# Kernel tuning notes

Hardware: AMD Instinct MI355X
Metric: run time of the kernel (lower is better)

Reference implementation:

```python
import jax, jax.numpy as jnp
import numpy as np

N_EMBD = 2048
N_HEAD = 16
HEAD_DIM = N_EMBD // N_HEAD
B, T = 4, 2048
EPS = 1e-5


def layer_norm(x, w, b):
    mu = jnp.mean(x, axis=-1, keepdims=True)
    var = jnp.var(x, axis=-1, keepdims=True)
    return (x - mu) * jax.lax.rsqrt(var + EPS) * w + b


def setup_inputs() -> dict:
    key = jax.random.key(0)
    ks = jax.random.split(key, 8)
    s = 0.02
    return {
        "x": jax.random.normal(ks[0], (B, T, N_EMBD), dtype=jnp.float32),
        "ln1_w": jnp.ones((N_EMBD,), jnp.float32),
        "ln1_b": jnp.zeros((N_EMBD,), jnp.float32),
        "attn_w": jax.random.normal(ks[1], (N_EMBD, 3 * N_EMBD), jnp.float32) * s,
        "attn_b": jnp.zeros((3 * N_EMBD,), jnp.float32),
        "ln2_w": jnp.ones((N_EMBD,), jnp.float32),
        "ln2_b": jnp.zeros((N_EMBD,), jnp.float32),
        "fc_w": jax.random.normal(ks[2], (N_EMBD, 4 * N_EMBD), jnp.float32) * s,
        "fc_b": jnp.zeros((4 * N_EMBD,), jnp.float32),
        "proj_w": jax.random.normal(ks[3], (4 * N_EMBD, N_EMBD), jnp.float32) * s,
        "proj_b": jnp.zeros((N_EMBD,), jnp.float32),
    }


def reference(x, ln1_w, ln1_b, attn_w, attn_b, ln2_w, ln2_b, fc_w, fc_b, proj_w, proj_b):
    b, t, c = x.shape
    # --- causal self-attention on ln_1(x); note: source Block has NO residual
    # and attention's c_proj is never invoked in the original forward. ---
    h = layer_norm(x, ln1_w, ln1_b)
    qkv = h @ attn_w + attn_b                      # [B,T,3C]
    q, k, v = jnp.split(qkv, 3, axis=-1)
    q = q.reshape(b, t, N_HEAD, HEAD_DIM)
    k = k.reshape(b, t, N_HEAD, HEAD_DIM)
    v = v.reshape(b, t, N_HEAD, HEAD_DIM)
    scale = 1.0 / np.sqrt(HEAD_DIM).astype(np.float32)
    scores = jnp.einsum("bqhd,bkhd->bhqk", q, k) * scale   # [B,H,T,T]
    causal = jnp.tril(jnp.ones((t, t), dtype=bool))
    scores = jnp.where(causal, scores, -jnp.inf)
    attn = jax.nn.softmax(scores, axis=-1)
    y = jnp.einsum("bhqk,bkhd->bqhd", attn, v).reshape(b, t, c)
    # --- MLP on ln_2(y); again no residual in the source Block ---
    h2 = layer_norm(y, ln2_w, ln2_b)
    out = jax.nn.gelu(h2 @ fc_w + fc_b, approximate=False) @ proj_w + proj_b
    return out
```

## Files before the change

kernel.cpp:

```cpp
#include <hip/hip_runtime.h>
#include <hip/hip_bf16.h>

typedef __attribute__((ext_vector_type(8))) short      bf16x8;
typedef __attribute__((ext_vector_type(4))) float      f32x4;
typedef __attribute__((ext_vector_type(8))) unsigned short u16x8;

__device__ __forceinline__ unsigned short f2bf(float f) {
    union { __hip_bfloat16 h; unsigned short u; } cv;
    cv.h = __float2bfloat16(f);
    return cv.u;
}
__device__ __forceinline__ float bf2f(unsigned short u) {
    union { float f; unsigned int i; } cv;
    cv.i = ((unsigned int)u) << 16;
    return cv.f;
}
__device__ __forceinline__ void gload_lds16(const void* g, void* l) {
    __builtin_amdgcn_global_load_lds(
        (const __attribute__((address_space(1))) void*)g,
        (__attribute__((address_space(3))) void*)l, 16, 0, 0);
}
__device__ __forceinline__ f32x4 mfma16(bf16x8 a, bf16x8 b, f32x4 c) {
    return __builtin_amdgcn_mfma_f32_16x16x32_bf16(a, b, c, 0, 0, 0);
}
__device__ __forceinline__ float gelu_f(float x) {
    return 0.5f * x * (1.0f + erff(x * 0.70710678118654752f));
}

#define VMCNT(N)  asm volatile("s_waitcnt vmcnt(" #N ")" ::: "memory")

template<int IN_BF16>
__global__ __launch_bounds__(256) void ln_kernel(const void* in, const float* w, const float* b,
                                                 unsigned short* out) {
    const int row = blockIdx.x;
    const int tid = threadIdx.x;
    float v[8];
    if constexpr (IN_BF16) {
        const unsigned short* p = (const unsigned short*)in + (size_t)row * 2048 + tid * 8;
        u16x8 raw = *(const u16x8*)p;
#pragma unroll
        for (int j = 0; j < 8; j++) v[j] = bf2f(raw[j]);
    } else {
        const float* p = (const float*)in + (size_t)row * 2048 + tid * 8;
        float4 a = ((const float4*)p)[0];
        float4 c = ((const float4*)p)[1];
        v[0] = a.x; v[1] = a.y; v[2] = a.z; v[3] = a.w;
        v[4] = c.x; v[5] = c.y; v[6] = c.z; v[7] = c.w;
    }
    float s = 0.f, ss = 0.f;
#pragma unroll
    for (int j = 0; j < 8; j++) { s += v[j]; ss += v[j] * v[j]; }
#pragma unroll
    for (int off = 32; off > 0; off >>= 1) {
        s  += __shfl_xor(s, off);
        ss += __shfl_xor(ss, off);
    }
    __shared__ float red[8];
    const int wid = tid >> 6, lane = tid & 63;
    if (lane == 0) { red[wid] = s; red[4 + wid] = ss; }
    __syncthreads();
    s  = red[0] + red[1] + red[2] + red[3];
    ss = red[4] + red[5] + red[6] + red[7];
    const float mean = s * (1.0f / 2048.0f);
    const float var  = ss * (1.0f / 2048.0f) - mean * mean;
    const float rstd = rsqrtf(var + 1e-5f);
    unsigned short* op = out + (size_t)row * 2048 + tid * 8;
    u16x8 ov;
#pragma unroll
    for (int j = 0; j < 8; j++) {
        int c = tid * 8 + j;
        ov[j] = f2bf((v[j] - mean) * rstd * w[c] + b[c]);
    }
    *(u16x8*)op = ov;
}

__global__ __launch_bounds__(256) void wt_kernel(const float* W, unsigned short* WT, int K, int N) {
    __shared__ unsigned short sm[32][33];
    const int n0 = blockIdx.x * 32, k0 = blockIdx.y * 32;
    const int tx = threadIdx.x, ty = threadIdx.y;
#pragma unroll
    for (int i = 0; i < 4; i++) {
        int k = ty + i * 8;
        sm[k][tx] = f2bf(W[(size_t)(k0 + k) * N + n0 + tx]);
    }
    __syncthreads();
#pragma unroll
    for (int i = 0; i < 4; i++) {
        int n = ty + i * 8;
        WT[(size_t)(n0 + n) * K + k0 + tx] = sm[tx][n];
    }
}

__global__ __launch_bounds__(256) void vt_kernel(const unsigned short* qkv, unsigned short* vT) {
    __shared__ unsigned short sm[32][33];
    const int t0 = blockIdx.x * 32, d0 = blockIdx.y * 32, bh = blockIdx.z;
    const int b = bh >> 4, h = bh & 15;
    const int tx = threadIdx.x, ty = threadIdx.y;
#pragma unroll
    for (int i = 0; i < 4; i++) {
        int t = ty + i * 8;
        sm[t][tx] = qkv[(size_t)(b * 2048 + t0 + t) * 6144 + 4096 + h * 128 + d0 + tx];
    }
    __syncthreads();
#pragma unroll
    for (int i = 0; i < 4; i++) {
        int d = ty + i * 8;
        vT[(size_t)(bh * 128 + d0 + d) * 2048 + t0 + tx] = sm[tx][d];
    }
}

template<int OUT_BF16, int ACT_GELU>
__global__ __launch_bounds__(512, 2) void gemm256(const unsigned short* __restrict__ A,
                                                  const unsigned short* __restrict__ BT,
                                                  const float* __restrict__ bias,
                                                  void* __restrict__ Cout,
                                                  int M, int N, int K) {
    __shared__ unsigned short As[2][256 * 64];
    __shared__ unsigned short Bs[2][256 * 64];
    const int tid = threadIdx.x;
    const int gx = gridDim.x;
    const int lin = blockIdx.y * gx + blockIdx.x;
    const int cpx = (gx * gridDim.y) >> 3;
    const int swz = (lin & 7) * cpx + (lin >> 3);
    const int n0 = (swz % gx) * 256, m0 = (swz / gx) * 256;

    const int wid = tid >> 6, lane = tid & 63;
    const int wr = wid >> 2, wc = wid & 3;
    const int lg = lane >> 4, l15 = lane & 15;
    const int nkt = K >> 6;

    const int sr = tid >> 3;
    const int scol = ((tid & 7) ^ (sr & 7)) * 8;
    const int sdst = tid * 8;

    auto stageA = [&](int ta, int h) {
        const unsigned short* g = A + (size_t)(m0 + h * 128 + sr) * K + ta * 64 + scol;
        unsigned short* d = &As[ta & 1][h * 8192 + sdst];
        gload_lds16(g, d);
        gload_lds16(g + (size_t)64 * K, d + 4096);
    };
    auto stageB = [&](int ta, int h) {
        const unsigned short* g = BT + (size_t)(n0 + h * 128 + sr) * K + ta * 64 + scol;
        unsigned short* d = &Bs[ta & 1][h * 8192 + sdst];
        gload_lds16(g, d);
        gload_lds16(g + (size_t)64 * K, d + 4096);
    };

    stageA(0, 0); stageA(0, 1); stageB(0, 0); stageB(0, 1);
    stageB(1, 0);
    VMCNT(2);
    __builtin_amdgcn_s_barrier();

    f32x4 acc[8][4] = {};
    const int lxor = l15 & 7;
    const int co0 = (lg ^ lxor) * 8;
    const int co1 = ((4 + lg) ^ lxor) * 8;
    const int aoff = wr * 8192;
    const int boff = (wc >> 1) * 8192 + (wc & 1) * 4096;

#define RD_A(P, MB, CO)                                                          \
    _Pragma("unroll") for (int i = 0; i < 4; i++)                                \
        af[i] = *(const bf16x8*)&P[aoff + (((MB) + i) * 16 + l15) * 64 + (CO)];
#define RD_B(DST, P, CO)                                                         \
    _Pragma("unroll") for (int n = 0; n < 4; n++)                                \
        DST[n] = *(const bf16x8*)&P[boff + (n * 16 + l15) * 64 + (CO)];
#define MM(MB, BQ)                                                               \
    __builtin_amdgcn_s_setprio(1);                                               \
    _Pragma("unroll") for (int i = 0; i < 4; i++)                                \
        _Pragma("unroll") for (int n = 0; n < 4; n++)                            \
            acc[(MB) + i][n] = mfma16(af[i], BQ[n], acc[(MB) + i][n]);           \
    __builtin_amdgcn_s_setprio(0);
#define BAR()  __builtin_amdgcn_s_barrier()
#define LGKM() asm volatile("s_waitcnt lgkmcnt(0)" ::: "memory")

    for (int it = 0, nit = nkt >> 1; it < nit; ++it) {
        const int T0 = it * 2, T1 = T0 + 1;
        const unsigned short* Ae = As[0];
        const unsigned short* Be = Bs[0];
        const unsigned short* Ao = As[1];
        const unsigned short* Bo = Bs[1];
        bf16x8 af[4], bq0[4], bq1[4];

        RD_A(Ae, 0, co0); RD_B(bq0, Be, co0);
        stageB(T1, 1);
        BAR(); LGKM(); MM(0, bq0); BAR();
        RD_A(Ae, 4, co0);
        stageA(T1, 0);
        BAR(); LGKM(); MM(4, bq0); BAR();
        RD_A(Ae, 0, co1); RD_B(bq1, Be, co1);
        stageA(T1, 1);
        BAR(); LGKM(); MM(0, bq1); BAR();
        RD_A(Ae, 4, co1);
        if (T0 + 2 < nkt) stageB(T0 + 2, 0);
        BAR(); LGKM(); MM(4, bq1); VMCNT(2); BAR();
        RD_A(Ao, 0, co0); RD_B(bq0, Bo, co0);
        if (T0 + 2 < nkt) stageB(T0 + 2, 1);
        BAR(); LGKM(); MM(0, bq0); BAR();
        RD_A(Ao, 4, co0);
        if (T0 + 2 < nkt) stageA(T0 + 2, 0);
        BAR(); LGKM(); MM(4, bq0); BAR();
        RD_A(Ao, 0, co1); RD_B(bq1, Bo, co1);
        if (T0 + 2 < nkt) stageA(T0 + 2, 1);
        BAR(); LGKM(); MM(0, bq1); BAR();
        RD_A(Ao, 4, co1);
        if (T1 + 2 < nkt) stageB(T1 + 2, 0);
        BAR(); LGKM(); MM(4, bq1); VMCNT(2); BAR();
    }
#undef RD_A
#undef RD_B
#undef MM
#undef BAR
#undef LGKM

#pragma unroll
    for (int n = 0; n < 4; n++) {
        const int col = n0 + wc * 64 + n * 16 + l15;
        const float bv = bias[col];
#pragma unroll
        for (int m = 0; m < 8; m++) {
            const int rbase = m0 + wr * 128 + m * 16 + lg * 4;
#pragma unroll
            for (int r = 0; r < 4; r++) {
                float v = acc[m][n][r] + bv;
                if (ACT_GELU) v = gelu_f(v);
                if (OUT_BF16)
                    ((unsigned short*)Cout)[(size_t)(rbase + r) * N + col] = f2bf(v);
                else
                    ((float*)Cout)[(size_t)(rbase + r) * N + col] = v;
            }
        }
    }
}

__global__ __launch_bounds__(256) void attn_kernel(const unsigned short* __restrict__ qkv,
                                                   const unsigned short* __restrict__ vT,
                                                   unsigned short* __restrict__ y) {
    __shared__ unsigned short Qs[64 * 128];
    __shared__ unsigned short Ks[64 * 128];
    __shared__ unsigned short VTs[128 * 64];
    const int pair = blockIdx.x, h = blockIdx.y, b = blockIdx.z;
    const int tid = threadIdx.x, wid = tid >> 6, lane = tid & 63;
    const int lg = lane >> 4, l15 = lane & 15;
    const float scale = 0.08838834764831845f;
    unsigned short* Ps = &Qs[wid * 1024];

    for (int pass = 0; pass < 2; pass++) {
        const int qt = (pass == 0) ? (31 - pair) : pair;
        __syncthreads();
#pragma unroll
        for (int i = 0; i < 4; i++) {
            int idx = tid + 256 * i;
            int row = idx >> 4, ch = idx & 15;
            const unsigned short* g = qkv + (size_t)(b * 2048 + qt * 64 + row) * 6144
                                      + h * 128 + ((ch ^ (row & 7)) * 8);
            gload_lds16(g, &Qs[idx * 8]);
        }
        __syncthreads();
        const int rq = wid * 16 + l15;
        bf16x8 qf[4];
#pragma unroll
        for (int c = 0; c < 4; c++)
            qf[c] = *(const bf16x8*)&Qs[rq * 128 + (((c * 4 + lg) ^ (rq & 7)) * 8)];

        float m_run[4], l_run[4];
#pragma unroll
        for (int r = 0; r < 4; r++) { m_run[r] = -1e30f; l_run[r] = 0.f; }
        f32x4 O[8] = {};

        const int nkb = qt + 1;
        for (int kb = 0; kb < nkb; kb++) {
            __syncthreads();
#pragma unroll
            for (int i = 0; i < 4; i++) {
                int idx = tid + 256 * i;
                int row = idx >> 4, ch = idx & 15;
                const unsigned short* g = qkv + (size_t)(b * 2048 + kb * 64 + row) * 6144
                                          + 2048 + h * 128 + ((ch ^ (row & 7)) * 8);
                gload_lds16(g, &Ks[idx * 8]);
            }
#pragma unroll
            for (int i = 0; i < 4; i++) {
                int idx = tid + 256 * i;
                int row = idx >> 3, ch = idx & 7;
                const unsigned short* g = vT + (size_t)((b * 16 + h) * 128 + row) * 2048
                                          + kb * 64 + ((ch ^ (row & 7)) * 8);
                gload_lds16(g, &VTs[idx * 8]);
            }
            __syncthreads();

            f32x4 S[4] = {};
#pragma unroll
            for (int n = 0; n < 4; n++) {
                const int rk = n * 16 + l15;
#pragma unroll
                for (int c = 0; c < 4; c++) {
                    bf16x8 kf = *(const bf16x8*)&Ks[rk * 128 + (((c * 4 + lg) ^ (rk & 7)) * 8)];
                    S[n] = mfma16(qf[c], kf, S[n]);
                }
            }

            const int qgb = qt * 64 + wid * 16 + lg * 4;
#pragma unroll
            for (int r = 0; r < 4; r++) {
                const int qg = qgb + r;
                float sv[4];
#pragma unroll
                for (int n = 0; n < 4; n++) {
                    const int kg = kb * 64 + n * 16 + l15;
                    sv[n] = (kg <= qg) ? S[n][r] * scale : -1e30f;
                }
                float mx = fmaxf(fmaxf(sv[0], sv[1]), fmaxf(sv[2], sv[3]));
                mx = fmaxf(mx, __shfl_xor(mx, 1));
                mx = fmaxf(mx, __shfl_xor(mx, 2));
                mx = fmaxf(mx, __shfl_xor(mx, 4));
                mx = fmaxf(mx, __shfl_xor(mx, 8));
                const float mnew = fmaxf(m_run[r], mx);
                const float f = __expf(m_run[r] - mnew);
                const float p0 = __expf(sv[0] - mnew), p1 = __expf(sv[1] - mnew);
                const float p2 = __expf(sv[2] - mnew), p3 = __expf(sv[3] - mnew);
                float rs = (p0 + p1) + (p2 + p3);
                rs += __shfl_xor(rs, 1);
                rs += __shfl_xor(rs, 2);
                rs += __shfl_xor(rs, 4);
                rs += __shfl_xor(rs, 8);
                l_run[r] = l_run[r] * f + rs;
                m_run[r] = mnew;
#pragma unroll
                for (int n2 = 0; n2 < 8; n2++) O[n2][r] *= f;
                const int prow = lg * 4 + r;
                const int pxor = (prow & 7) << 3;
                Ps[(prow * 64 + l15) ^ pxor]      = f2bf(p0);
                Ps[(prow * 64 + 16 + l15) ^ pxor] = f2bf(p1);
                Ps[(prow * 64 + 32 + l15) ^ pxor] = f2bf(p2);
                Ps[(prow * 64 + 48 + l15) ^ pxor] = f2bf(p3);
            }

#pragma unroll
            for (int kk = 0; kk < 2; kk++) {
                bf16x8 pf = *(const bf16x8*)&Ps[l15 * 64 + (((kk * 4 + lg) ^ (l15 & 7)) * 8)];
#pragma unroll
                for (int n2 = 0; n2 < 8; n2++) {
                    const int rv = n2 * 16 + l15;
                    bf16x8 vf = *(const bf16x8*)&VTs[rv * 64 + (((kk * 4 + lg) ^ (rv & 7)) * 8)];
                    O[n2] = mfma16(pf, vf, O[n2]);
                }
            }
        }

#pragma unroll
        for (int r = 0; r < 4; r++) {
            const float inv = 1.0f / l_run[r];
            const size_t row = (size_t)(b * 2048 + qt * 64 + wid * 16 + lg * 4 + r);
#pragma unroll
            for (int n2 = 0; n2 < 8; n2++)
                y[row * 2048 + h * 128 + n2 * 16 + l15] = f2bf(O[n2][r] * inv);
        }
    }
}

extern "C" void kernel_launch(void* const* d_in, const int* in_sizes, int n_in,
                              void* d_out, int out_size, void* d_ws, size_t ws_size,
                              hipStream_t stream) {
    const float* x      = (const float*)d_in[0];
    const float* ln1_w  = (const float*)d_in[1];
    const float* ln1_b  = (const float*)d_in[2];
    const float* attn_w = (const float*)d_in[3];
    const float* attn_b = (const float*)d_in[4];
    const float* ln2_w  = (const float*)d_in[5];
    const float* ln2_b  = (const float*)d_in[6];
    const float* fc_w   = (const float*)d_in[7];
    const float* fc_b   = (const float*)d_in[8];
    const float* proj_w = (const float*)d_in[9];
    const float* proj_b = (const float*)d_in[10];
    float* out = (float*)d_out;

    char* ws = (char*)d_ws;
    const size_t MB = 1024ull * 1024ull;
    unsigned short* Wt   = (unsigned short*)(ws + 0);
    unsigned short* X1   = (unsigned short*)(ws + 32 * MB);
    unsigned short* X2   = (unsigned short*)(ws + 64 * MB);
    unsigned short* QKV  = (unsigned short*)(ws + 96 * MB);
    unsigned short* VT   = (unsigned short*)(ws + 192 * MB);
    unsigned short* Abuf = (unsigned short*)(ws + 96 * MB);

    ln_kernel<0><<<8192, 256, 0, stream>>>(x, ln1_w, ln1_b, X1);
    wt_kernel<<<dim3(6144 / 32, 2048 / 32), dim3(32, 8), 0, stream>>>(attn_w, Wt, 2048, 6144);
    gemm256<1, 0><<<dim3(24, 32), 512, 0, stream>>>(X1, Wt, attn_b, QKV, 8192, 6144, 2048);
    vt_kernel<<<dim3(64, 4, 64), dim3(32, 8), 0, stream>>>(QKV, VT);
    attn_kernel<<<dim3(16, 16, 4), 256, 0, stream>>>(QKV, VT, X2);
    ln_kernel<1><<<8192, 256, 0, stream>>>(X2, ln2_w, ln2_b, X1);
    wt_kernel<<<dim3(8192 / 32, 2048 / 32), dim3(32, 8), 0, stream>>>(fc_w, Wt, 2048, 8192);
    gemm256<1, 1><<<dim3(32, 32), 512, 0, stream>>>(X1, Wt, fc_b, Abuf, 8192, 8192, 2048);
    wt_kernel<<<dim3(2048 / 32, 8192 / 32), dim3(32, 8), 0, stream>>>(proj_w, Wt, 8192, 2048);
    gemm256<0, 0><<<dim3(8, 32), 512, 0, stream>>>(Abuf, Wt, proj_b, out, 8192, 2048, 8192);
}
```

Before: 1.075 ms.

## Simplify GEMM main loop to one barrier per K-tile double buffering

Replaces the finely interleaved 8-phase pipeline, which staged quarter tiles between per-subtile MFMA groups with a barrier around each, with a simple loop. Each K-tile now issues the full next-tile prefetch up front, runs all MFMAs from LDS, then waits on vmcnt(0) and takes a single barrier. This drops many barriers per iteration. The cost is coarser overlap of global-to-LDS loads with compute, a full vmcnt(0) drain each tile, and LDS reads no longer fenced by explicit waits before MFMAs.

```diff
diff --git a/kernel.cpp b/kernel.cpp
--- a/kernel.cpp
+++ b/kernel.cpp
@@ -28,6 +28,8 @@
 }
 
 #define VMCNT(N)  asm volatile("s_waitcnt vmcnt(" #N ")" ::: "memory")
+#define LGKM()    asm volatile("s_waitcnt lgkmcnt(0)" ::: "memory")
+#define BAR()     __builtin_amdgcn_s_barrier()
 
 template<int IN_BF16>
 __global__ __launch_bounds__(256) void ln_kernel(const void* in, const float* w, const float* b,
@@ -131,25 +133,23 @@
 
     const int sr = tid >> 3;
     const int scol = ((tid & 7) ^ (sr & 7)) * 8;
-    const int sdst = tid * 8;
 
     auto stageA = [&](int ta, int h) {
         const unsigned short* g = A + (size_t)(m0 + h * 128 + sr) * K + ta * 64 + scol;
-        unsigned short* d = &As[ta & 1][h * 8192 + sdst];
+        unsigned short* d = &As[ta & 1][h * 8192 + tid * 8];
         gload_lds16(g, d);
         gload_lds16(g + (size_t)64 * K, d + 4096);
     };
     auto stageB = [&](int ta, int h) {
         const unsigned short* g = BT + (size_t)(n0 + h * 128 + sr) * K + ta * 64 + scol;
-        unsigned short* d = &Bs[ta & 1][h * 8192 + sdst];
+        unsigned short* d = &Bs[ta & 1][h * 8192 + tid * 8];
         gload_lds16(g, d);
         gload_lds16(g + (size_t)64 * K, d + 4096);
     };
 
     stageA(0, 0); stageA(0, 1); stageB(0, 0); stageB(0, 1);
-    stageB(1, 0);
-    VMCNT(2);
-    __builtin_amdgcn_s_barrier();
+    VMCNT(0);
+    BAR();
 
     f32x4 acc[8][4] = {};
     const int lxor = l15 & 7;
@@ -161,56 +161,36 @@
 #define RD_A(P, MB, CO)                                                          \
     _Pragma("unroll") for (int i = 0; i < 4; i++)                                \
         af[i] = *(const bf16x8*)&P[aoff + (((MB) + i) * 16 + l15) * 64 + (CO)];
-#define RD_B(DST, P, CO)                                                         \
+#define RD_B(P, CO)                                                              \
     _Pragma("unroll") for (int n = 0; n < 4; n++)                                \
-        DST[n] = *(const bf16x8*)&P[boff + (n * 16 + l15) * 64 + (CO)];
-#define MM(MB, BQ)                                                               \
+        bq[n] = *(const bf16x8*)&P[boff + (n * 16 + l15) * 64 + (CO)];
+#define MM(MB)                                                                   \
     __builtin_amdgcn_s_setprio(1);                                               \
-    _Pragma("unroll") for (int i = 0; i < 4; i++)                                \
+    _Pragma("unroll") for (int i = 0; i < 4; i++) {                              \
         _Pragma("unroll") for (int n = 0; n < 4; n++)                            \
-            acc[(MB) + i][n] = mfma16(af[i], BQ[n], acc[(MB) + i][n]);           \
+            acc[(MB) + i][n] = mfma16(af[i], bq[n], acc[(MB) + i][n]);           \
+    }                                                                            \
     __builtin_amdgcn_s_setprio(0);
-#define BAR()  __builtin_amdgcn_s_barrier()
-#define LGKM() asm volatile("s_waitcnt lgkmcnt(0)" ::: "memory")
-
-    for (int it = 0, nit = nkt >> 1; it < nit; ++it) {
-        const int T0 = it * 2, T1 = T0 + 1;
-        const unsigned short* Ae = As[0];
-        const unsigned short* Be = Bs[0];
-        const unsigned short* Ao = As[1];
-        const unsigned short* Bo = Bs[1];
-        bf16x8 af[4], bq0[4], bq1[4];
-
-        RD_A(Ae, 0, co0); RD_B(bq0, Be, co0);
-        stageB(T1, 1);
-        BAR(); LGKM(); MM(0, bq0); BAR();
-        RD_A(Ae, 4, co0);
-        stageA(T1, 0);
-        BAR(); LGKM(); MM(4, bq0); BAR();
-        RD_A(Ae, 0, co1); RD_B(bq1, Be, co1);
-        stageA(T1, 1);
-        BAR(); LGKM(); MM(0, bq1); BAR();
-        RD_A(Ae, 4, co1);
-        if (T0 + 2 < nkt) stageB(T0 + 2, 0);
-        BAR(); LGKM(); MM(4, bq1); VMCNT(2); BAR();
-        RD_A(Ao, 0, co0); RD_B(bq0, Bo, co0);
-        if (T0 + 2 < nkt) stageB(T0 + 2, 1);
-        BAR(); LGKM(); MM(0, bq0); BAR();
-        RD_A(Ao, 4, co0);
-        if (T0 + 2 < nkt) stageA(T0 + 2, 0);
-        BAR(); LGKM(); MM(4, bq0); BAR();
-        RD_A(Ao, 0, co1); RD_B(bq1, Bo, co1);
-        if (T0 + 2 < nkt) stageA(T0 + 2, 1);
-        BAR(); LGKM(); MM(0, bq1); BAR();
-        RD_A(Ao, 4, co1);
-        if (T1 + 2 < nkt) stageB(T1 + 2, 0);
-        BAR(); LGKM(); MM(4, bq1); VMCNT(2); BAR();
+
+    for (int t = 0; t < nkt; ++t) {
+        const unsigned short* Ap = As[t & 1];
+        const unsigned short* Bp = Bs[t & 1];
+        if (t + 1 < nkt) {
+            stageA(t + 1, 0); stageA(t + 1, 1);
+            stageB(t + 1, 0); stageB(t + 1, 1);
+        }
+        bf16x8 af[4], bq[4];
+        RD_B(Bp, co0); RD_A(Ap, 0, co0); MM(0);
+        RD_A(Ap, 4, co0);               MM(4);
+        RD_B(Bp, co1); RD_A(Ap, 0, co1); MM(0);
+        RD_A(Ap, 4, co1);               MM(4);
+        LGKM();
+        if (t + 1 < nkt) VMCNT(0);
+        BAR();
     }
 #undef RD_A
 #undef RD_B
 #undef MM
-#undef BAR
-#undef LGKM
 
 #pragma unroll
     for (int n = 0; n < 4; n++) {
```

New measurement: 1.100 ms. 1.02x slower.
